# Kernel tuning notes

Hardware: AMD Instinct MI355X
Metric: run time of the kernel (lower is better)

## Reference

```python
import jax, jax.numpy as jnp
import numpy as np
from jax import lax


def _conv1d(x, w):
    # x: (B, L, C), w: (K, C, C), SAME padding (flax nnx.Conv default)
    return lax.conv_general_dilated(x, w, (1,), 'SAME', dimension_numbers=('NWC', 'WIO', 'NWC'))


def _message_passing(x, w, vertical, reverse):
    # x: (B, H, W, C). Sequential SCNN update along H (vertical) or W (horizontal):
    #   slice_i += relu(conv1d(slice_{i-1}))
    if not vertical:
        x = jnp.swapaxes(x, 1, 2)  # scan axis -> axis 1
    if reverse:
        x = x[:, ::-1]
    first = x[:, 0]                       # (B, Wd, C)
    rest = jnp.moveaxis(x[:, 1:], 1, 0)   # (L-1, B, Wd, C)

    def step(prev, row):
        new = row + jax.nn.relu(_conv1d(prev, w))
        return new, new

    _, out = lax.scan(step, first, rest)
    x = jnp.concatenate([first[:, None], jnp.moveaxis(out, 0, 1)], axis=1)
    if reverse:
        x = x[:, ::-1]
    if not vertical:
        x = jnp.swapaxes(x, 1, 2)
    return x


def _bn(x, scale, bias, eps=1e-5):
    # flax nnx.BatchNorm in training mode: batch stats over (B, H, W)
    mean = x.mean((0, 1, 2))
    var = x.var((0, 1, 2))
    return (x - mean) * lax.rsqrt(var + eps) * scale + bias


def reference(features, w_conv1, bn1_scale, bn1_bias, w_conv2, bn2_scale, bn2_bias,
              w_mp_vf, w_mp_vr, w_mp_hf, w_mp_hr, w_seg, b_seg,
              w_fc1, b_fc1, w_fc2, b_fc2):
    dn = ('NHWC', 'HWIO', 'NHWC')
    # dilated 3x3 conv (pad 4, dilation 4) -> BN -> relu
    x = lax.conv_general_dilated(features, w_conv1, (1, 1), [(4, 4), (4, 4)],
                                 rhs_dilation=(4, 4), dimension_numbers=dn)
    x = jax.nn.relu(_bn(x, bn1_scale, bn1_bias))
    # 1x1 conv -> BN -> relu
    x = lax.conv_general_dilated(x, w_conv2, (1, 1), 'SAME', dimension_numbers=dn)
    x = jax.nn.relu(_bn(x, bn2_scale, bn2_bias))
    # four SCNN message-passing directions (sequential scans)
    x = _message_passing(x, w_mp_vf, True, False)
    x = _message_passing(x, w_mp_vr, True, True)
    x = _message_passing(x, w_mp_hf, False, False)
    x = _message_passing(x, w_mp_hr, False, True)
    # seg head: dropout (deterministic -> identity) + 1x1 conv with bias
    x = lax.conv_general_dilated(x, w_seg, (1, 1), 'SAME', dimension_numbers=dn) + b_seg
    b, h, w, f = x.shape
    logits_seg = jax.image.resize(x, (b, h * 8, w * 8, f), method='linear')
    # existence head: softmax -> avg_pool 2x2 -> flatten -> MLP
    p = jax.nn.softmax(x, axis=-1)
    p = p.reshape(b, h // 2, 2, w // 2, 2, f).mean((2, 4))
    p = p.reshape(b, -1)  # (B, (h/2)*(w/2)*f) = (B, 4500)
    z = jax.nn.relu(p @ w_fc1 + b_fc1)
    logits_ext = z @ w_fc2 + b_fc2
    return logits_seg, logits_ext


def setup_inputs() -> dict:
    key = jax.random.key(0)
    ks = jax.random.split(key, 10)
    B, H, W, C = 16, 36, 100, 512
    n_lanes = 4
    s = 0.05
    return {
        'features': jax.random.normal(ks[0], (B, H, W, C), jnp.float32),
        'w_conv1': jax.random.normal(ks[1], (3, 3, 512, 1024), jnp.float32) * s,
        'bn1_scale': jnp.ones((1024,), jnp.float32),
        'bn1_bias': jnp.zeros((1024,), jnp.float32),
        'w_conv2': jax.random.normal(ks[2], (1, 1, 1024, 128), jnp.float32) * s,
        'bn2_scale': jnp.ones((128,), jnp.float32),
        'bn2_bias': jnp.zeros((128,), jnp.float32),
        'w_mp_vf': jax.random.normal(ks[3], (9, 128, 128), jnp.float32) * 0.02,
        'w_mp_vr': jax.random.normal(ks[4], (9, 128, 128), jnp.float32) * 0.02,
        'w_mp_hf': jax.random.normal(ks[5], (9, 128, 128), jnp.float32) * 0.02,
        'w_mp_hr': jax.random.normal(ks[6], (9, 128, 128), jnp.float32) * 0.02,
        'w_seg': jax.random.normal(ks[7], (1, 1, 128, n_lanes + 1), jnp.float32) * s,
        'b_seg': jnp.zeros((n_lanes + 1,), jnp.float32),
        'w_fc1': jax.random.normal(ks[8], (4500, 128), jnp.float32) * s,
        'b_fc1': jnp.zeros((128,), jnp.float32),
        'w_fc2': jax.random.normal(ks[9], (128, n_lanes), jnp.float32) * s,
        'b_fc2': jnp.zeros((n_lanes,), jnp.float32),
    }
```

## Files before the change

kernel.cpp:

```cpp
#include <hip/hip_runtime.h>
#include <hip/hip_bf16.h>

#define NB 16
#define NPOS 57600

typedef short bf16x8 __attribute__((ext_vector_type(8)));
typedef float f32x4 __attribute__((ext_vector_type(4)));

__device__ __forceinline__ float bf2f(unsigned short u) {
  union { unsigned int i; float f; } c; c.i = ((unsigned int)u) << 16; return c.f;
}
__device__ __forceinline__ unsigned short f2bf(float f) {
  union { float f; unsigned int i; } c; c.f = f;
  unsigned int x = c.i;
  x += 0x7fffu + ((x >> 16) & 1u);
  return (unsigned short)(x >> 16);
}
__device__ __forceinline__ unsigned int pk2(float lo, float hi) {
  return (unsigned int)f2bf(lo) | ((unsigned int)f2bf(hi) << 16);
}

__device__ __forceinline__ void gload_lds16(const void* g, void* l) {
  __builtin_amdgcn_global_load_lds(
      (const __attribute__((address_space(1))) unsigned int*)(g),
      (__attribute__((address_space(3))) unsigned int*)(l), 16, 0, 0);
}

__global__ __launch_bounds__(256) void convert_w1t(const float* __restrict__ w,
                                                   unsigned short* __restrict__ wt)
{
  int idx = blockIdx.x * 256 + threadIdx.x;
  int n = idx & 1023;
  int k0 = (idx >> 10) * 8;
  unsigned int o[4];
#pragma unroll
  for (int j = 0; j < 4; ++j) {
    float lo = w[(long)(k0 + 2*j)     * 1024 + n];
    float hi = w[(long)(k0 + 2*j + 1) * 1024 + n];
    o[j] = pk2(lo, hi);
  }
  *(uint4*)(wt + (long)n * 4608 + k0) = make_uint4(o[0], o[1], o[2], o[3]);
}

__global__ __launch_bounds__(256) void convert_w2t(const float* __restrict__ w,
                                                   unsigned short* __restrict__ wt)
{
  int idx = blockIdx.x * 256 + threadIdx.x;
  int n = idx & 127;
  int k0 = (idx >> 7) * 8;
  unsigned int o[4];
#pragma unroll
  for (int j = 0; j < 4; ++j) {
    float lo = w[(long)(k0 + 2*j)     * 128 + n];
    float hi = w[(long)(k0 + 2*j + 1) * 128 + n];
    o[j] = pk2(lo, hi);
  }
  *(uint4*)(wt + (long)n * 1024 + k0) = make_uint4(o[0], o[1], o[2], o[3]);
}

__global__ __launch_bounds__(256) void convert_wmp(const float* __restrict__ w,
                                                   unsigned short* __restrict__ wt)
{
  int idx = blockIdx.x * 256 + threadIdx.x;
  if (idx >= 18432) return;
  int co = idx & 127;
  int kg = idx >> 7;
  int k0 = kg * 8;
  int tap = k0 >> 7, ci0 = k0 & 127;
  const float* src = w + (long)tap * 16384 + (long)ci0 * 128 + co;
  unsigned int o[4];
#pragma unroll
  for (int j = 0; j < 4; ++j)
    o[j] = pk2(src[(2*j) * 128], src[(2*j+1) * 128]);
  *(uint4*)(wt + (long)co * 1152 + k0) = make_uint4(o[0], o[1], o[2], o[3]);
}

__global__ __launch_bounds__(256) void pad_features(const float* __restrict__ src,
                                                    unsigned short* __restrict__ dst)
{
  long idx = (long)blockIdx.x * 256 + threadIdx.x;
  if (idx >= 16L * 44 * 108 * 64) return;
  int c8 = (int)(idx & 63);
  long pos = idx >> 6;
  int wp = (int)(pos % 108); pos /= 108;
  int hp = (int)(pos % 44);
  int b  = (int)(pos / 44);
  uint4 o = make_uint4(0u, 0u, 0u, 0u);
  if (hp >= 4 && hp < 40 && wp >= 4 && wp < 104) {
    const float* s = src + (((long)b * 36 + (hp - 4)) * 100 + (wp - 4)) * 512 + c8 * 8;
    float4 v0 = *(const float4*)s;
    float4 v1 = *(const float4*)(s + 4);
    o = make_uint4(pk2(v0.x, v0.y), pk2(v0.z, v0.w), pk2(v1.x, v1.y), pk2(v1.z, v1.w));
  }
  *(uint4*)(dst + (((long)b * 44 + hp) * 108 + wp) * 512 + c8 * 8) = o;
}

__global__ __launch_bounds__(256) void conv1_mfma2(
    const unsigned short* __restrict__ inp,
    const unsigned short* __restrict__ w1t,
    unsigned short* __restrict__ x1)
{
  __shared__ unsigned short Al[128 * 32];
  __shared__ unsigned short Bl[128 * 32];
  const int tid  = threadIdx.x;
  const int lane = tid & 63;
  const int wave = tid >> 6;
  const int wm = wave >> 1, wn = wave & 1;
  const int bid  = blockIdx.x;
  const int nbid = (bid & 7) * 450 + (bid >> 3);
  const int n0 = (nbid & 7) * 128;
  const int m0 = (nbid >> 3) * 128;

  long aoff[2];
  const unsigned short* bsrc[2];
#pragma unroll
  for (int q = 0; q < 2; ++q) {
    int e = q * 256 + tid;
    int row = e >> 2;
    int kl  = (e & 3) * 8;
    int m = m0 + row;
    int w = m % 100, h = (m / 100) % 36, b = m / 3600;
    aoff[q] = (((long)b * 44 + h + 4) * 108 + (w + 4)) * 512 + kl;
    bsrc[q] = w1t + (long)(n0 + row) * 4608 + kl;
  }

  f32x4 acc[4][4];
#pragma unroll
  for (int i = 0; i < 4; ++i)
#pragma unroll
    for (int j = 0; j < 4; ++j) acc[i][j] = (f32x4){0.f, 0.f, 0.f, 0.f};

  const int fr = lane & 15;
  const int fk = (lane >> 4) * 8;
  const unsigned short* Alrd = Al + (wm * 64 + fr) * 32 + fk;
  const unsigned short* Blrd = Bl + (wn * 64 + fr) * 32 + fk;

  for (int k0 = 0; k0 < 4608; k0 += 32) {
    const int tap = k0 >> 9;
    const int ci0 = k0 & 511;
    const int dh = (tap / 3) * 4 - 4, dw = (tap % 3) * 4 - 4;
    const long delta = (long)(dh * 108 + dw) * 512 + ci0;
    __syncthreads();
#pragma unroll
    for (int q = 0; q < 2; ++q) {
      gload_lds16(inp + aoff[q] + delta, Al + (q * 256 + tid) * 8);
      gload_lds16(bsrc[q] + k0,          Bl + (q * 256 + tid) * 8);
    }
    __syncthreads();
    bf16x8 af[4], bfr[4];
#pragma unroll
    for (int m = 0; m < 4; ++m) af[m]  = *(const bf16x8*)(Alrd + m * 16 * 32);
#pragma unroll
    for (int n = 0; n < 4; ++n) bfr[n] = *(const bf16x8*)(Blrd + n * 16 * 32);
#pragma unroll
    for (int m = 0; m < 4; ++m)
#pragma unroll
      for (int n = 0; n < 4; ++n)
        acc[m][n] = __builtin_amdgcn_mfma_f32_16x16x32_bf16(af[m], bfr[n], acc[m][n], 0, 0, 0);
  }
  const int r0 = (lane >> 4) * 4;
#pragma unroll
  for (int m = 0; m < 4; ++m) {
    int row = m0 + wm * 64 + m * 16 + r0;
#pragma unroll
    for (int n = 0; n < 4; ++n) {
      int col = n0 + wn * 64 + n * 16 + fr;
#pragma unroll
      for (int j = 0; j < 4; ++j)
        x1[(long)(row + j) * 1024 + col] = f2bf(acc[m][n][j]);
    }
  }
}

__global__ __launch_bounds__(256) void conv1_mfma(
    const float* __restrict__ in,
    const unsigned short* __restrict__ w1t,
    unsigned short* __restrict__ x1)
{
  __shared__ unsigned short Al[128 * 32];
  __shared__ unsigned short Bl[128 * 32];
  const int tid  = threadIdx.x;
  const int lane = tid & 63;
  const int wave = tid >> 6;
  const int wm = wave >> 1, wn = wave & 1;
  const int m0 = blockIdx.y * 128;
  const int n0 = blockIdx.x * 128;

  int akl[2], ab_[2], ah_[2], aw_[2];
  const unsigned short* bsrc[2];
#pragma unroll
  for (int q = 0; q < 2; ++q) {
    int e = q * 256 + tid;
    int row = e >> 2;
    akl[q]  = (e & 3) * 8;
    int m = m0 + row;
    aw_[q] = m % 100;
    ah_[q] = (m / 100) % 36;
    ab_[q] = m / 3600;
    bsrc[q] = w1t + (long)(n0 + row) * 4608 + akl[q];
  }

  f32x4 acc[4][4];
#pragma unroll
  for (int i = 0; i < 4; ++i)
#pragma unroll
    for (int j = 0; j < 4; ++j) acc[i][j] = (f32x4){0.f, 0.f, 0.f, 0.f};

  const int fr = lane & 15;
  const int fk = (lane >> 4) * 8;
  const unsigned short* Alrd = Al + (wm * 64 + fr) * 32 + fk;
  const unsigned short* Blrd = Bl + (wn * 64 + fr) * 32 + fk;

  for (int k0 = 0; k0 < 4608; k0 += 32) {
    const int tap = k0 >> 9;
    const int ci0 = k0 & 511;
    const int dh = (tap / 3) * 4 - 4, dw = (tap % 3) * 4 - 4;
    unsigned int apk[2][4];
#pragma unroll
    for (int q = 0; q < 2; ++q) {
      int ih = ah_[q] + dh, iw = aw_[q] + dw;
      if ((unsigned)ih < 36u && (unsigned)iw < 100u) {
        const float* s = in + ((((long)ab_[q] * 36 + ih) * 100 + iw) << 9) + ci0 + akl[q];
        float4 v0 = *(const float4*)s;
        float4 v1 = *(const float4*)(s + 4);
        apk[q][0] = pk2(v0.x, v0.y); apk[q][1] = pk2(v0.z, v0.w);
        apk[q][2] = pk2(v1.x, v1.y); apk[q][3] = pk2(v1.z, v1.w);
      } else {
        apk[q][0] = apk[q][1] = apk[q][2] = apk[q][3] = 0u;
      }
    }
    __syncthreads();
#pragma unroll
    for (int q = 0; q < 2; ++q) {
      *(uint4*)(Al + (q * 256 + tid) * 8) = *(uint4*)apk[q];
      gload_lds16(bsrc[q] + k0, Bl + (q * 256 + tid) * 8);
    }
    __syncthreads();
    bf16x8 af[4], bfr[4];
#pragma unroll
    for (int m = 0; m < 4; ++m) af[m]  = *(const bf16x8*)(Alrd + m * 16 * 32);
#pragma unroll
    for (int n = 0; n < 4; ++n) bfr[n] = *(const bf16x8*)(Blrd + n * 16 * 32);
#pragma unroll
    for (int m = 0; m < 4; ++m)
#pragma unroll
      for (int n = 0; n < 4; ++n)
        acc[m][n] = __builtin_amdgcn_mfma_f32_16x16x32_bf16(af[m], bfr[n], acc[m][n], 0, 0, 0);
  }
  const int r0 = (lane >> 4) * 4;
#pragma unroll
  for (int m = 0; m < 4; ++m) {
    int row = m0 + wm * 64 + m * 16 + r0;
#pragma unroll
    for (int n = 0; n < 4; ++n) {
      int col = n0 + wn * 64 + n * 16 + fr;
#pragma unroll
      for (int j = 0; j < 4; ++j)
        x1[(long)(row + j) * 1024 + col] = f2bf(acc[m][n][j]);
    }
  }
}

__global__ __launch_bounds__(256) void gemm_mfma_128(
    const unsigned short* __restrict__ A,
    const unsigned short* __restrict__ Bt,
    float* __restrict__ C, int K)
{
  __shared__ unsigned short Al[128 * 32];
  __shared__ unsigned short Bl[128 * 32];
  const int tid  = threadIdx.x;
  const int lane = tid & 63;
  const int wave = tid >> 6;
  const int wm = wave >> 1, wn = wave & 1;
  const int m0 = blockIdx.x * 128;

  const unsigned short* asrc[2];
  const unsigned short* bsrc[2];
#pragma unroll
  for (int q = 0; q < 2; ++q) {
    int e = q * 256 + tid;
    int row = e >> 2;
    int kl  = (e & 3) * 8;
    asrc[q] = A  + (long)(m0 + row) * K + kl;
    bsrc[q] = Bt + (long)row * K + kl;
  }

  f32x4 acc[4][4];
#pragma unroll
  for (int i = 0; i < 4; ++i)
#pragma unroll
    for (int j = 0; j < 4; ++j) acc[i][j] = (f32x4){0.f, 0.f, 0.f, 0.f};

  const int fr = lane & 15;
  const int fk = (lane >> 4) * 8;
  const unsigned short* Alrd = Al + (wm * 64 + fr) * 32 + fk;
  const unsigned short* Blrd = Bl + (wn * 64 + fr) * 32 + fk;

  for (int k0 = 0; k0 < K; k0 += 32) {
    __syncthreads();
#pragma unroll
    for (int q = 0; q < 2; ++q) {
      gload_lds16(asrc[q] + k0, Al + (q * 256 + tid) * 8);
      gload_lds16(bsrc[q] + k0, Bl + (q * 256 + tid) * 8);
    }
    __syncthreads();
    bf16x8 af[4], bfr[4];
#pragma unroll
    for (int m = 0; m < 4; ++m) af[m]  = *(const bf16x8*)(Alrd + m * 16 * 32);
#pragma unroll
    for (int n = 0; n < 4; ++n) bfr[n] = *(const bf16x8*)(Blrd + n * 16 * 32);
#pragma unroll
    for (int m = 0; m < 4; ++m)
#pragma unroll
      for (int n = 0; n < 4; ++n)
        acc[m][n] = __builtin_amdgcn_mfma_f32_16x16x32_bf16(af[m], bfr[n], acc[m][n], 0, 0, 0);
  }
  const int r0 = (lane >> 4) * 4;
#pragma unroll
  for (int m = 0; m < 4; ++m) {
    int row = m0 + wm * 64 + m * 16 + r0;
#pragma unroll
    for (int n = 0; n < 4; ++n) {
      int col = wn * 64 + n * 16 + fr;
#pragma unroll
      for (int j = 0; j < 4; ++j)
        C[(long)(row + j) * 128 + col] = acc[m][n][j];
    }
  }
}

__global__ __launch_bounds__(256) void stats1(const unsigned short* __restrict__ x1,
                                              float* __restrict__ sum, float* __restrict__ ssq)
{
  const int tid = threadIdx.x;
  const int c0 = tid * 4;
  float s0=0,s1=0,s2=0,s3=0,q0=0,q1=0,q2=0,q3=0;
  for (int r = blockIdx.x; r < NPOS; r += gridDim.x) {
    uint2 v = *(const uint2*)(x1 + (long)r * 1024 + c0);
    float f0 = bf2f(v.x & 0xffffu), f1 = bf2f(v.x >> 16);
    float f2 = bf2f(v.y & 0xffffu), f3 = bf2f(v.y >> 16);
    s0 += f0; q0 += f0*f0;  s1 += f1; q1 += f1*f1;
    s2 += f2; q2 += f2*f2;  s3 += f3; q3 += f3*f3;
  }
  atomicAdd(&sum[c0+0], s0); atomicAdd(&ssq[c0+0], q0);
  atomicAdd(&sum[c0+1], s1); atomicAdd(&ssq[c0+1], q1);
  atomicAdd(&sum[c0+2], s2); atomicAdd(&ssq[c0+2], q2);
  atomicAdd(&sum[c0+3], s3); atomicAdd(&ssq[c0+3], q3);
}

__global__ void finalize_bn(const float* __restrict__ sum, const float* __restrict__ ssq,
                            const float* __restrict__ scale, const float* __restrict__ bias,
                            float* __restrict__ ab, int C, float invN)
{
  int c = blockIdx.x * blockDim.x + threadIdx.x;
  if (c >= C) return;
  float mean = sum[c] * invN;
  float var  = ssq[c] * invN - mean * mean;
  float a = scale[c] * rsqrtf(var + 1e-5f);
  ab[c] = a;
  ab[C + c] = bias[c] - mean * a;
}

__global__ __launch_bounds__(256) void bnrelu_x1(unsigned short* __restrict__ x1,
                                                 const float* __restrict__ ab)
{
  long base = ((long)blockIdx.x * 256 + threadIdx.x) * 8;
  int c0 = (int)(base & 1023);
  uint4 v = *(uint4*)(x1 + base);
  unsigned int w[4] = {v.x, v.y, v.z, v.w};
  unsigned int o[4];
#pragma unroll
  for (int j = 0; j < 4; ++j) {
    int c = c0 + j * 2;
    float lo = bf2f((unsigned short)(w[j] & 0xffffu));
    float hi = bf2f((unsigned short)(w[j] >> 16));
    lo = fmaxf(fmaf(lo, ab[c],     ab[1024 + c]),     0.f);
    hi = fmaxf(fmaf(hi, ab[c + 1], ab[1024 + c + 1]), 0.f);
    o[j] = pk2(lo, hi);
  }
  *(uint4*)(x1 + base) = make_uint4(o[0], o[1], o[2], o[3]);
}

__global__ __launch_bounds__(256) void stats2(const float* __restrict__ x2,
                                              float* __restrict__ sum, float* __restrict__ ssq)
{
  const int c = threadIdx.x & 127;
  const int g = threadIdx.x >> 7;
  float s = 0.f, q = 0.f;
  for (int r = blockIdx.x * 2 + g; r < NPOS; r += gridDim.x * 2) {
    float v = x2[(long)r * 128 + c];
    s += v; q += v * v;
  }
  atomicAdd(&sum[c], s); atomicAdd(&ssq[c], q);
}

__global__ __launch_bounds__(256) void apply_bn(float* __restrict__ x, const float* __restrict__ ab)
{
  int idx = (blockIdx.x * 256 + threadIdx.x) * 4;
  if (idx >= NPOS * 128) return;
  int c = idx & 127;
  float4 v = *(float4*)(x + idx);
  v.x = fmaxf(fmaf(v.x, ab[c+0], ab[128+c+0]), 0.f);
  v.y = fmaxf(fmaf(v.y, ab[c+1], ab[128+c+1]), 0.f);
  v.z = fmaxf(fmaf(v.z, ab[c+2], ab[128+c+2]), 0.f);
  v.w = fmaxf(fmaf(v.w, ab[c+3], ab[128+c+3]), 0.f);
  *(float4*)(x + idx) = v;
}

#define MPROWS 120
#define MPBUF (MPROWS * 128)
template<int MT, int MH>
__global__ __launch_bounds__(512, 2) void mp_fused2(
    float* __restrict__ x2, const unsigned short* __restrict__ wt,
    const int L, const int posStride, const int rowStride,
    const int i0, const int di, const int nsteps)
{
  __shared__ unsigned short rowbuf[2 * MPBUF];
  __shared__ float xch[MT * 8 * 16 * 17];
  const int tid  = threadIdx.x;
  const int lane = tid & 63;
  const int wave = tid >> 6;
  const int ng   = wave & 3;
  const int kh   = wave >> 2;
  const int fr   = lane & 15;
  const int ks   = lane >> 4;
  float* xb = x2 + (long)blockIdx.x * 460800;

  for (int i = tid; i < (2 * MPBUF) / 8; i += 512)
    *(uint4*)(rowbuf + i * 8) = make_uint4(0u, 0u, 0u, 0u);

  const unsigned short* wb = wt + (long)(ng * 32 + fr) * 1152 + kh * 576 + ks * 8;
  bf16x8 bfrag[2][18];
#pragma unroll
  for (int nt = 0; nt < 2; ++nt)
#pragma unroll
    for (int kk = 0; kk < 18; ++kk)
      bfrag[nt][kk] = *(const bf16x8*)(wb + nt * 16 * 1152 + kk * 32);

  __syncthreads();
  for (int e = tid * 4; e < L * 128; e += 2048) {
    int w = e >> 7, c = e & 127;
    float4 v = *(const float4*)(xb + (long)i0 * rowStride + (long)w * posStride + c);
    int br = w + 4;
    int byte = (br * 256 + c * 2) ^ ((br & 7) << 4);
    *(uint2*)((char*)rowbuf + byte) = make_uint2(pk2(v.x, v.y), pk2(v.z, v.w));
  }
  __syncthreads();

#define MP_EPI(mt)                                                             \
  _Pragma("unroll")                                                            \
  for (int nt = 0; nt < 2; ++nt) {                                             \
    const int col = ng * 32 + nt * 16 + fr;                                    \
    const float* src = &xch[(((mt) * 8 + ng * 2 + nt) * 16) * 17];             \
    _Pragma("unroll")                                                          \
    for (int j = 0; j < 4; ++j) {                                              \
      const int m = (mt) * 16 + ks * 4 + j;                                    \
      if (m < L) {                                                             \
        float v = acc[mt][nt][j] + src[(ks * 4 + j) * 17 + fr];                \
        long off = (long)i * rowStride + (long)m * posStride + col;            \
        float nv = xb[off] + fmaxf(v, 0.f);                                    \
        xb[off] = nv;                                                          \
        int br = m + 4;                                                        \
        int byte = (br * 256 + col * 2) ^ ((br & 7) << 4);                     \
        *(unsigned short*)(nxtb + byte) = f2bf(nv);                            \
      }                                                                        \
    }                                                                          \
  }

  for (int s = 1; s <= nsteps; ++s) {
    const char* curb = (const char*)rowbuf + (((s & 1) ^ 1) * MPBUF) * 2;
    char* nxtb = (char*)rowbuf + ((s & 1) * MPBUF) * 2;
    const int i = i0 + s * di;

    f32x4 acc[MT][2];
#pragma unroll
    for (int mt = 0; mt < MT; ++mt) {
      acc[mt][0] = (f32x4){0.f, 0.f, 0.f, 0.f};
      acc[mt][1] = (f32x4){0.f, 0.f, 0.f, 0.f};
    }

#pragma unroll
    for (int kk = 0; kk < 18; ++kk) {
      const int k0 = kh * 576 + kk * 32;
      const int tap = k0 >> 7;
      const int colb = ((k0 & 127) + ks * 8) * 2;
      const int br0 = fr + tap;
      const int byte0 = (br0 * 256 + colb) ^ ((br0 & 7) << 4);
#pragma unroll
      for (int mt = 0; mt < MT; ++mt) {
        bf16x8 af = *(const bf16x8*)(curb + byte0 + mt * 4096);
        acc[mt][0] = __builtin_amdgcn_mfma_f32_16x16x32_bf16(af, bfrag[0][kk], acc[mt][0], 0, 0, 0);
        acc[mt][1] = __builtin_amdgcn_mfma_f32_16x16x32_bf16(af, bfrag[1][kk], acc[mt][1], 0, 0, 0);
      }
    }

    if (kh == 0) {
#pragma unroll
      for (int mt = MH; mt < MT; ++mt) {
#pragma unroll
        for (int nt = 0; nt < 2; ++nt) {
          float* dst = &xch[((mt * 8 + ng * 2 + nt) * 16) * 17];
#pragma unroll
          for (int j = 0; j < 4; ++j)
            dst[(ks * 4 + j) * 17 + fr] = acc[mt][nt][j];
        }
      }
    } else {
#pragma unroll
      for (int mt = 0; mt < MH; ++mt) {
#pragma unroll
        for (int nt = 0; nt < 2; ++nt) {
          float* dst = &xch[((mt * 8 + ng * 2 + nt) * 16) * 17];
#pragma unroll
          for (int j = 0; j < 4; ++j)
            dst[(ks * 4 + j) * 17 + fr] = acc[mt][nt][j];
        }
      }
    }
    __syncthreads();
    if (kh == 0) {
#pragma unroll
      for (int mt = 0; mt < MH; ++mt) { MP_EPI(mt) }
    } else {
#pragma unroll
      for (int mt = MH; mt < MT; ++mt) { MP_EPI(mt) }
    }
    __syncthreads();
  }
#undef MP_EPI
}

__global__ __launch_bounds__(256) void seg_head(
    const float* __restrict__ xn, const float* __restrict__ w_seg,
    const float* __restrict__ b_seg, float* __restrict__ logits)
{
  __shared__ float ws[128 * 5];
  __shared__ float xs[32][129];
  const int tid = threadIdx.x;
  for (int i = tid; i < 640; i += 256) ws[i] = w_seg[i];
  const int pos0 = blockIdx.x * 32;
  for (int idx = tid; idx < 32 * 32; idx += 256) {
    int r = idx >> 5, q = idx & 31;
    float4 v = *(const float4*)(xn + (long)(pos0 + r) * 128 + q * 4);
    xs[r][q*4+0]=v.x; xs[r][q*4+1]=v.y; xs[r][q*4+2]=v.z; xs[r][q*4+3]=v.w;
  }
  __syncthreads();
  int r = tid >> 3, f = tid & 7;
  if (f < 5) {
    float acc = b_seg[f];
#pragma unroll 4
    for (int ci = 0; ci < 128; ++ci) acc = fmaf(xs[r][ci], ws[ci*5 + f], acc);
    logits[(long)(pos0 + r) * 5 + f] = acc;
  }
}

__global__ __launch_bounds__(256) void softpool(const float* __restrict__ logits, float* __restrict__ p)
{
  int idx = blockIdx.x * 256 + threadIdx.x;
  if (idx >= 16 * 18 * 50) return;
  int ww = idx % 50, hh = (idx / 50) % 18, b = idx / 900;
  float avg[5] = {0,0,0,0,0};
#pragma unroll
  for (int i = 0; i < 2; ++i)
#pragma unroll
    for (int j = 0; j < 2; ++j) {
      const float* L = logits + ((long)((b*36 + hh*2 + i) * 100) + ww*2 + j) * 5;
      float l0=L[0], l1=L[1], l2=L[2], l3=L[3], l4=L[4];
      float m = fmaxf(fmaxf(fmaxf(l0,l1), fmaxf(l2,l3)), l4);
      float e0=expf(l0-m), e1=expf(l1-m), e2=expf(l2-m), e3=expf(l3-m), e4=expf(l4-m);
      float inv = 1.f / (e0+e1+e2+e3+e4);
      avg[0] += e0*inv; avg[1] += e1*inv; avg[2] += e2*inv; avg[3] += e3*inv; avg[4] += e4*inv;
    }
  float* dst = p + (long)b * 4500 + (hh * 50 + ww) * 5;
#pragma unroll
  for (int f = 0; f < 5; ++f) dst[f] = avg[f] * 0.25f;
}

__global__ __launch_bounds__(128) void fc1_kernel(
    const float* __restrict__ p, const float* __restrict__ w,
    const float* __restrict__ bias, float* __restrict__ z)
{
  __shared__ float ps[4500];
  const int b = blockIdx.x, tid = threadIdx.x;
  for (int i = tid; i < 4500; i += 128) ps[i] = p[(long)b * 4500 + i];
  __syncthreads();
  float acc = bias[tid];
#pragma unroll 4
  for (int m = 0; m < 4500; ++m) acc = fmaf(ps[m], w[(long)m * 128 + tid], acc);
  z[b * 128 + tid] = fmaxf(acc, 0.f);
}

__global__ void fc2_kernel(const float* __restrict__ z, const float* __restrict__ w,
                           const float* __restrict__ bias, float* __restrict__ out)
{
  int t = threadIdx.x;
  if (t >= 64) return;
  int b = t >> 2, j = t & 3;
  float acc = bias[j];
#pragma unroll 4
  for (int n = 0; n < 128; ++n) acc = fmaf(z[b*128 + n], w[n*4 + j], acc);
  out[b*4 + j] = acc;
}

__global__ __launch_bounds__(256) void resize_bilinear(
    const float* __restrict__ logits, float* __restrict__ out)
{
  int idx = blockIdx.x * 256 + threadIdx.x;
  if (idx >= 18432000) return;
  int f = idx % 5;
  int t = idx / 5;
  int ow = t % 800; t /= 800;
  int oh = t % 288;
  int b = t / 288;
  float sh = (oh + 0.5f) * 0.125f - 0.5f;
  float sw = (ow + 0.5f) * 0.125f - 0.5f;
  int h0 = (int)floorf(sh); float fh = sh - (float)h0;
  int w0 = (int)floorf(sw); float fw = sw - (float)w0;
  int h1 = min(h0 + 1, 35); h0 = max(h0, 0);
  int w1 = min(w0 + 1, 99); w0 = max(w0, 0);
  const float* Lb = logits + (long)b * 36 * 100 * 5 + f;
  float v00 = Lb[(h0*100 + w0)*5], v01 = Lb[(h0*100 + w1)*5];
  float v10 = Lb[(h1*100 + w0)*5], v11 = Lb[(h1*100 + w1)*5];
  float v = (1.f-fh) * ((1.f-fw)*v00 + fw*v01) + fh * ((1.f-fw)*v10 + fw*v11);
  out[idx] = v;
}

extern "C" void kernel_launch(void* const* d_in, const int* in_sizes, int n_in,
                              void* d_out, int out_size, void* d_ws, size_t ws_size,
                              hipStream_t stream)
{
  (void)in_sizes; (void)n_in; (void)out_size;
  const float* features = (const float*)d_in[0];
  const float* w_conv1  = (const float*)d_in[1];
  const float* bn1_s    = (const float*)d_in[2];
  const float* bn1_b    = (const float*)d_in[3];
  const float* w_conv2  = (const float*)d_in[4];
  const float* bn2_s    = (const float*)d_in[5];
  const float* bn2_b    = (const float*)d_in[6];
  const float* w_vf     = (const float*)d_in[7];
  const float* w_vr     = (const float*)d_in[8];
  const float* w_hf     = (const float*)d_in[9];
  const float* w_hr     = (const float*)d_in[10];
  const float* w_seg    = (const float*)d_in[11];
  const float* b_seg    = (const float*)d_in[12];
  const float* w_fc1    = (const float*)d_in[13];
  const float* b_fc1    = (const float*)d_in[14];
  const float* w_fc2    = (const float*)d_in[15];
  const float* b_fc2    = (const float*)d_in[16];

  char* ws = (char*)d_ws;
  unsigned short* x1  = (unsigned short*)ws;
  unsigned short* w1t = (unsigned short*)(ws + 117964800);
  float* x2     = (float*)(ws + 117964800);
  float* logits = (float*)(ws + 147456000);
  unsigned short* wtmp = (unsigned short*)(ws + 147456000);
  float* pbuf   = (float*)(ws + 148608000);
  float* zbuf   = (float*)(ws + 148896000);
  float* stats  = (float*)(ws + 148904192);
  float* ab1    = (float*)(ws + 148913408);
  float* ab2    = (float*)(ws + 148921600);
  unsigned short* w2t = (unsigned short*)(ws + 148922624);
  unsigned short* in_pad = (unsigned short*)(ws + 149184768);
  const bool use_pad = ws_size >= 227041536ULL;
  float* outf   = (float*)d_out;

  hipMemsetAsync(stats, 0, 2304 * sizeof(float), stream);
  convert_w1t<<<2304, 256, 0, stream>>>(w_conv1, w1t);
  convert_w2t<<<64, 256, 0, stream>>>(w_conv2, w2t);
  convert_wmp<<<72, 256, 0, stream>>>(w_vf, wtmp + 0 * 147456);
  convert_wmp<<<72, 256, 0, stream>>>(w_vr, wtmp + 1 * 147456);
  convert_wmp<<<72, 256, 0, stream>>>(w_hf, wtmp + 2 * 147456);
  convert_wmp<<<72, 256, 0, stream>>>(w_hr, wtmp + 3 * 147456);

  if (use_pad) {
    pad_features<<<19008, 256, 0, stream>>>(features, in_pad);
    conv1_mfma2<<<3600, 256, 0, stream>>>(in_pad, w1t, x1);
  } else {
    conv1_mfma<<<dim3(8, 450), 256, 0, stream>>>(features, w1t, x1);
  }
  stats1<<<512, 256, 0, stream>>>(x1, stats, stats + 1024);
  finalize_bn<<<4, 256, 0, stream>>>(stats, stats + 1024, bn1_s, bn1_b, ab1, 1024, 1.0f/57600.0f);
  bnrelu_x1<<<28800, 256, 0, stream>>>(x1, ab1);
  gemm_mfma_128<<<450, 256, 0, stream>>>(x1, w2t, x2, 1024);
  stats2<<<256, 256, 0, stream>>>(x2, stats + 2048, stats + 2176);
  finalize_bn<<<1, 128, 0, stream>>>(stats + 2048, stats + 2176, bn2_s, bn2_b, ab2, 128, 1.0f/57600.0f);
  apply_bn<<<7200, 256, 0, stream>>>(x2, ab2);

  mp_fused2<7,3><<<NB, 512, 0, stream>>>(x2, wtmp + 0 * 147456, 100, 128,   12800, 0,  +1, 35);
  mp_fused2<7,3><<<NB, 512, 0, stream>>>(x2, wtmp + 1 * 147456, 100, 128,   12800, 35, -1, 35);
  mp_fused2<3,1><<<NB, 512, 0, stream>>>(x2, wtmp + 2 * 147456, 36,  12800, 128,   0,  +1, 99);
  mp_fused2<3,1><<<NB, 512, 0, stream>>>(x2, wtmp + 3 * 147456, 36,  12800, 128,   99, -1, 99);

  seg_head<<<1800, 256, 0, stream>>>(x2, w_seg, b_seg, logits);
  softpool<<<57, 256, 0, stream>>>(logits, pbuf);
  fc1_kernel<<<16, 128, 0, stream>>>(pbuf, w_fc1, b_fc1, zbuf);
  fc2_kernel<<<1, 64, 0, stream>>>(zbuf, w_fc2, b_fc2, outf + 18432000);
  resize_bilinear<<<72000, 256, 0, stream>>>(logits, outf);
}
```

Measured before the change: 3.555 ms.

## Split message-passing work over M tiles instead of K halves, stream weights per tap

The sequential message-passing kernel previously split the K dimension across two wave groups and combined partial sums through a shared-memory exchange with an extra barrier each step, while holding all weight fragments in registers. It now splits the output rows (M tiles) between the two wave groups, so each wave accumulates the full K and writes its own epilogue, which removes the exchange buffer and one barrier per step. Weights are reloaded from global/L2 every step with tap-level double buffering rather than kept resident in registers, and the launch bound no longer requests two blocks per CU. The trade-offs are repeated weight traffic on the serial critical path and uneven M splits (4/3 and 2/1) that leave some waves with more MFMA work.

```diff
diff --git a/kernel.cpp b/kernel.cpp
--- a/kernel.cpp
+++ b/kernel.cpp
@@ -409,34 +409,26 @@
 
 #define MPROWS 120
 #define MPBUF (MPROWS * 128)
-template<int MT, int MH>
-__global__ __launch_bounds__(512, 2) void mp_fused2(
+template<int MT, int MG0>
+__global__ __launch_bounds__(512) void mp_fused3(
     float* __restrict__ x2, const unsigned short* __restrict__ wt,
     const int L, const int posStride, const int rowStride,
     const int i0, const int di, const int nsteps)
 {
+  constexpr int MG1 = MT - MG0;
+  constexpr int NMT = (MG0 > MG1) ? MG0 : MG1;
   __shared__ unsigned short rowbuf[2 * MPBUF];
-  __shared__ float xch[MT * 8 * 16 * 17];
   const int tid  = threadIdx.x;
   const int lane = tid & 63;
   const int wave = tid >> 6;
   const int ng   = wave & 3;
-  const int kh   = wave >> 2;
+  const int mg   = wave >> 2;
   const int fr   = lane & 15;
   const int ks   = lane >> 4;
   float* xb = x2 + (long)blockIdx.x * 460800;
 
   for (int i = tid; i < (2 * MPBUF) / 8; i += 512)
     *(uint4*)(rowbuf + i * 8) = make_uint4(0u, 0u, 0u, 0u);
-
-  const unsigned short* wb = wt + (long)(ng * 32 + fr) * 1152 + kh * 576 + ks * 8;
-  bf16x8 bfrag[2][18];
-#pragma unroll
-  for (int nt = 0; nt < 2; ++nt)
-#pragma unroll
-    for (int kk = 0; kk < 18; ++kk)
-      bfrag[nt][kk] = *(const bf16x8*)(wb + nt * 16 * 1152 + kk * 32);
-
   __syncthreads();
   for (int e = tid * 4; e < L * 128; e += 2048) {
     int w = e >> 7, c = e & 127;
@@ -447,18 +439,18 @@
   }
   __syncthreads();
 
-#define MP_EPI(mt)                                                             \
+  const unsigned short* wb = wt + (long)(ng * 32 + fr) * 1152 + ks * 8;
+
+#define MP_EPI(MTA, pi)                                                        \
   _Pragma("unroll")                                                            \
   for (int nt = 0; nt < 2; ++nt) {                                             \
     const int col = ng * 32 + nt * 16 + fr;                                    \
-    const float* src = &xch[(((mt) * 8 + ng * 2 + nt) * 16) * 17];             \
     _Pragma("unroll")                                                          \
     for (int j = 0; j < 4; ++j) {                                              \
-      const int m = (mt) * 16 + ks * 4 + j;                                    \
+      const int m = (MTA) * 16 + ks * 4 + j;                                   \
       if (m < L) {                                                             \
-        float v = acc[mt][nt][j] + src[(ks * 4 + j) * 17 + fr];                \
         long off = (long)i * rowStride + (long)m * posStride + col;            \
-        float nv = xb[off] + fmaxf(v, 0.f);                                    \
+        float nv = xb[off] + fmaxf(acc[pi][nt][j], 0.f);                       \
         xb[off] = nv;                                                          \
         int br = m + 4;                                                        \
         int byte = (br * 256 + col * 2) ^ ((br & 7) << 4);                     \
@@ -472,58 +464,63 @@
     char* nxtb = (char*)rowbuf + ((s & 1) * MPBUF) * 2;
     const int i = i0 + s * di;
 
-    f32x4 acc[MT][2];
-#pragma unroll
-    for (int mt = 0; mt < MT; ++mt) {
+    f32x4 acc[NMT][2];
+#pragma unroll
+    for (int mt = 0; mt < NMT; ++mt) {
       acc[mt][0] = (f32x4){0.f, 0.f, 0.f, 0.f};
       acc[mt][1] = (f32x4){0.f, 0.f, 0.f, 0.f};
     }
 
-#pragma unroll
-    for (int kk = 0; kk < 18; ++kk) {
-      const int k0 = kh * 576 + kk * 32;
-      const int tap = k0 >> 7;
-      const int colb = ((k0 & 127) + ks * 8) * 2;
-      const int br0 = fr + tap;
-      const int byte0 = (br0 * 256 + colb) ^ ((br0 & 7) << 4);
-#pragma unroll
-      for (int mt = 0; mt < MT; ++mt) {
-        bf16x8 af = *(const bf16x8*)(curb + byte0 + mt * 4096);
-        acc[mt][0] = __builtin_amdgcn_mfma_f32_16x16x32_bf16(af, bfrag[0][kk], acc[mt][0], 0, 0, 0);
-        acc[mt][1] = __builtin_amdgcn_mfma_f32_16x16x32_bf16(af, bfrag[1][kk], acc[mt][1], 0, 0, 0);
+    bf16x8 wbuf[2][2][4];
+#pragma unroll
+    for (int nt = 0; nt < 2; ++nt)
+#pragma unroll
+      for (int q = 0; q < 4; ++q)
+        wbuf[0][nt][q] = *(const bf16x8*)(wb + (long)nt * 16 * 1152 + q * 32);
+
+#pragma unroll
+    for (int tap = 0; tap < 9; ++tap) {
+      constexpr int B0 = 0;
+      const int cur = tap & 1;
+      const int nxt = cur ^ 1;
+      if (tap < 8) {
+#pragma unroll
+        for (int nt = 0; nt < 2; ++nt)
+#pragma unroll
+          for (int q = 0; q < 4; ++q)
+            wbuf[nxt][nt][q] =
+              *(const bf16x8*)(wb + (long)nt * 16 * 1152 + (tap + 1) * 128 + q * 32);
       }
-    }
-
-    if (kh == 0) {
-#pragma unroll
-      for (int mt = MH; mt < MT; ++mt) {
-#pragma unroll
-        for (int nt = 0; nt < 2; ++nt) {
-          float* dst = &xch[((mt * 8 + ng * 2 + nt) * 16) * 17];
-#pragma unroll
-          for (int j = 0; j < 4; ++j)
-            dst[(ks * 4 + j) * 17 + fr] = acc[mt][nt][j];
+      (void)B0;
+#pragma unroll
+      for (int q = 0; q < 4; ++q) {
+        const int colb = (q * 32 + ks * 8) * 2;
+        const int br0 = fr + tap;
+        const int byte0 = (br0 * 256 + colb) ^ ((br0 & 7) << 4);
+        if (mg == 0) {
+#pragma unroll
+          for (int mt = 0; mt < MG0; ++mt) {
+            bf16x8 af = *(const bf16x8*)(curb + byte0 + mt * 4096);
+            acc[mt][0] = __builtin_amdgcn_mfma_f32_16x16x32_bf16(af, wbuf[cur][0][q], acc[mt][0], 0, 0, 0);
+            acc[mt][1] = __builtin_amdgcn_mfma_f32_16x16x32_bf16(af, wbuf[cur][1][q], acc[mt][1], 0, 0, 0);
+          }
+        } else {
+#pragma unroll
+          for (int mt = 0; mt < MG1; ++mt) {
+            bf16x8 af = *(const bf16x8*)(curb + byte0 + (MG0 + mt) * 4096);
+            acc[mt][0] = __builtin_amdgcn_mfma_f32_16x16x32_bf16(af, wbuf[cur][0][q], acc[mt][0], 0, 0, 0);
+            acc[mt][1] = __builtin_amdgcn_mfma_f32_16x16x32_bf16(af, wbuf[cur][1][q], acc[mt][1], 0, 0, 0);
+          }
         }
       }
+    }
+
+    if (mg == 0) {
+#pragma unroll
+      for (int mt = 0; mt < MG0; ++mt) { MP_EPI(mt, mt) }
     } else {
 #pragma unroll
-      for (int mt = 0; mt < MH; ++mt) {
-#pragma unroll
-        for (int nt = 0; nt < 2; ++nt) {
-          float* dst = &xch[((mt * 8 + ng * 2 + nt) * 16) * 17];
-#pragma unroll
-          for (int j = 0; j < 4; ++j)
-            dst[(ks * 4 + j) * 17 + fr] = acc[mt][nt][j];
-        }
-      }
-    }
-    __syncthreads();
-    if (kh == 0) {
-#pragma unroll
-      for (int mt = 0; mt < MH; ++mt) { MP_EPI(mt) }
-    } else {
-#pragma unroll
-      for (int mt = MH; mt < MT; ++mt) { MP_EPI(mt) }
+      for (int mt = 0; mt < MG1; ++mt) { MP_EPI(MG0 + mt, mt) }
     }
     __syncthreads();
   }
@@ -686,10 +683,10 @@
   finalize_bn<<<1, 128, 0, stream>>>(stats + 2048, stats + 2176, bn2_s, bn2_b, ab2, 128, 1.0f/57600.0f);
   apply_bn<<<7200, 256, 0, stream>>>(x2, ab2);
 
-  mp_fused2<7,3><<<NB, 512, 0, stream>>>(x2, wtmp + 0 * 147456, 100, 128,   12800, 0,  +1, 35);
-  mp_fused2<7,3><<<NB, 512, 0, stream>>>(x2, wtmp + 1 * 147456, 100, 128,   12800, 35, -1, 35);
-  mp_fused2<3,1><<<NB, 512, 0, stream>>>(x2, wtmp + 2 * 147456, 36,  12800, 128,   0,  +1, 99);
-  mp_fused2<3,1><<<NB, 512, 0, stream>>>(x2, wtmp + 3 * 147456, 36,  12800, 128,   99, -1, 99);
+  mp_fused3<7,4><<<NB, 512, 0, stream>>>(x2, wtmp + 0 * 147456, 100, 128,   12800, 0,  +1, 35);
+  mp_fused3<7,4><<<NB, 512, 0, stream>>>(x2, wtmp + 1 * 147456, 100, 128,   12800, 35, -1, 35);
+  mp_fused3<3,2><<<NB, 512, 0, stream>>>(x2, wtmp + 2 * 147456, 36,  12800, 128,   0,  +1, 99);
+  mp_fused3<3,2><<<NB, 512, 0, stream>>>(x2, wtmp + 3 * 147456, 36,  12800, 128,   99, -1, 99);
 
   seg_head<<<1800, 256, 0, stream>>>(x2, w_seg, b_seg, logits);
   softpool<<<57, 256, 0, stream>>>(logits, pbuf);
```

Measured after the change: 5.997 ms. 68.7% more time.

## Halve message-passing block to 4 waves, each computing 64 output channels

Applied to the files above, without the earlier changes.

The SCNN message-passing kernel drops from 8 waves to 4 per block. Each wave now covers 64 output columns (4 N-tiles) and one K half, so every A fragment read from LDS feeds 4 MFMAs instead of 2, which cuts LDS traffic per MFMA. Weight fragments are no longer held in registers for the whole kernel; they are reloaded from global memory/cache at every K step, to make room for the larger accumulator set. The intent is to lower LDS and barrier overhead in this latency-bound sequential scan, but with half the waves there is less latency hiding and extra weight loads every step.

```diff
diff --git a/kernel.cpp b/kernel.cpp
--- a/kernel.cpp
+++ b/kernel.cpp
@@ -409,36 +409,27 @@
 
 #define MPROWS 120
 #define MPBUF (MPROWS * 128)
-template<int MT, int MH>
-__global__ __launch_bounds__(512, 2) void mp_fused2(
+template<int MT, int ME0>
+__global__ __launch_bounds__(256) void mp_fused5(
     float* __restrict__ x2, const unsigned short* __restrict__ wt,
     const int L, const int posStride, const int rowStride,
     const int i0, const int di, const int nsteps)
 {
   __shared__ unsigned short rowbuf[2 * MPBUF];
-  __shared__ float xch[MT * 8 * 16 * 17];
+  __shared__ float xch[MT][2][4][16][17];
   const int tid  = threadIdx.x;
   const int lane = tid & 63;
   const int wave = tid >> 6;
-  const int ng   = wave & 3;
-  const int kh   = wave >> 2;
+  const int ng   = wave & 1;
+  const int kg   = wave >> 1;
   const int fr   = lane & 15;
   const int ks   = lane >> 4;
   float* xb = x2 + (long)blockIdx.x * 460800;
 
-  for (int i = tid; i < (2 * MPBUF) / 8; i += 512)
+  for (int i = tid; i < (2 * MPBUF) / 8; i += 256)
     *(uint4*)(rowbuf + i * 8) = make_uint4(0u, 0u, 0u, 0u);
-
-  const unsigned short* wb = wt + (long)(ng * 32 + fr) * 1152 + kh * 576 + ks * 8;
-  bf16x8 bfrag[2][18];
-#pragma unroll
-  for (int nt = 0; nt < 2; ++nt)
-#pragma unroll
-    for (int kk = 0; kk < 18; ++kk)
-      bfrag[nt][kk] = *(const bf16x8*)(wb + nt * 16 * 1152 + kk * 32);
-
   __syncthreads();
-  for (int e = tid * 4; e < L * 128; e += 2048) {
+  for (int e = tid * 4; e < L * 128; e += 1024) {
     int w = e >> 7, c = e & 127;
     float4 v = *(const float4*)(xb + (long)i0 * rowStride + (long)w * posStride + c);
     int br = w + 4;
@@ -447,16 +438,17 @@
   }
   __syncthreads();
 
+  const unsigned short* wb = wt + (long)(ng * 64 + fr) * 1152 + kg * 576 + ks * 8;
+
 #define MP_EPI(mt)                                                             \
   _Pragma("unroll")                                                            \
-  for (int nt = 0; nt < 2; ++nt) {                                             \
-    const int col = ng * 32 + nt * 16 + fr;                                    \
-    const float* src = &xch[(((mt) * 8 + ng * 2 + nt) * 16) * 17];             \
+  for (int nt = 0; nt < 4; ++nt) {                                             \
+    const int col = ng * 64 + nt * 16 + fr;                                    \
     _Pragma("unroll")                                                          \
     for (int j = 0; j < 4; ++j) {                                              \
       const int m = (mt) * 16 + ks * 4 + j;                                    \
       if (m < L) {                                                             \
-        float v = acc[mt][nt][j] + src[(ks * 4 + j) * 17 + fr];                \
+        float v = acc[mt][nt][j] + xch[mt][ng][nt][ks * 4 + j][fr];            \
         long off = (long)i * rowStride + (long)m * posStride + col;            \
         float nv = xb[off] + fmaxf(v, 0.f);                                    \
         xb[off] = nv;                                                          \
@@ -472,58 +464,56 @@
     char* nxtb = (char*)rowbuf + ((s & 1) * MPBUF) * 2;
     const int i = i0 + s * di;
 
-    f32x4 acc[MT][2];
-#pragma unroll
-    for (int mt = 0; mt < MT; ++mt) {
-      acc[mt][0] = (f32x4){0.f, 0.f, 0.f, 0.f};
-      acc[mt][1] = (f32x4){0.f, 0.f, 0.f, 0.f};
-    }
+    f32x4 acc[MT][4];
+#pragma unroll
+    for (int mt = 0; mt < MT; ++mt)
+#pragma unroll
+      for (int nt = 0; nt < 4; ++nt) acc[mt][nt] = (f32x4){0.f, 0.f, 0.f, 0.f};
 
 #pragma unroll
     for (int kk = 0; kk < 18; ++kk) {
-      const int k0 = kh * 576 + kk * 32;
+      const int k0 = kg * 576 + kk * 32;
       const int tap = k0 >> 7;
       const int colb = ((k0 & 127) + ks * 8) * 2;
+      bf16x8 bf[4];
+#pragma unroll
+      for (int nt = 0; nt < 4; ++nt)
+        bf[nt] = *(const bf16x8*)(wb + (long)nt * 16 * 1152 + kk * 32);
       const int br0 = fr + tap;
       const int byte0 = (br0 * 256 + colb) ^ ((br0 & 7) << 4);
 #pragma unroll
       for (int mt = 0; mt < MT; ++mt) {
         bf16x8 af = *(const bf16x8*)(curb + byte0 + mt * 4096);
-        acc[mt][0] = __builtin_amdgcn_mfma_f32_16x16x32_bf16(af, bfrag[0][kk], acc[mt][0], 0, 0, 0);
-        acc[mt][1] = __builtin_amdgcn_mfma_f32_16x16x32_bf16(af, bfrag[1][kk], acc[mt][1], 0, 0, 0);
+#pragma unroll
+        for (int nt = 0; nt < 4; ++nt)
+          acc[mt][nt] = __builtin_amdgcn_mfma_f32_16x16x32_bf16(af, bf[nt], acc[mt][nt], 0, 0, 0);
       }
     }
 
-    if (kh == 0) {
-#pragma unroll
-      for (int mt = MH; mt < MT; ++mt) {
-#pragma unroll
-        for (int nt = 0; nt < 2; ++nt) {
-          float* dst = &xch[((mt * 8 + ng * 2 + nt) * 16) * 17];
+    if (kg == 0) {
+#pragma unroll
+      for (int mt = ME0; mt < MT; ++mt)
+#pragma unroll
+        for (int nt = 0; nt < 4; ++nt)
 #pragma unroll
           for (int j = 0; j < 4; ++j)
-            dst[(ks * 4 + j) * 17 + fr] = acc[mt][nt][j];
-        }
-      }
+            xch[mt][ng][nt][ks * 4 + j][fr] = acc[mt][nt][j];
     } else {
 #pragma unroll
-      for (int mt = 0; mt < MH; ++mt) {
-#pragma unroll
-        for (int nt = 0; nt < 2; ++nt) {
-          float* dst = &xch[((mt * 8 + ng * 2 + nt) * 16) * 17];
+      for (int mt = 0; mt < ME0; ++mt)
+#pragma unroll
+        for (int nt = 0; nt < 4; ++nt)
 #pragma unroll
           for (int j = 0; j < 4; ++j)
-            dst[(ks * 4 + j) * 17 + fr] = acc[mt][nt][j];
-        }
-      }
-    }
-    __syncthreads();
-    if (kh == 0) {
-#pragma unroll
-      for (int mt = 0; mt < MH; ++mt) { MP_EPI(mt) }
+            xch[mt][ng][nt][ks * 4 + j][fr] = acc[mt][nt][j];
+    }
+    __syncthreads();
+    if (kg == 0) {
+#pragma unroll
+      for (int mt = 0; mt < ME0; ++mt) { MP_EPI(mt) }
     } else {
 #pragma unroll
-      for (int mt = MH; mt < MT; ++mt) { MP_EPI(mt) }
+      for (int mt = ME0; mt < MT; ++mt) { MP_EPI(mt) }
     }
     __syncthreads();
   }
@@ -686,10 +676,10 @@
   finalize_bn<<<1, 128, 0, stream>>>(stats + 2048, stats + 2176, bn2_s, bn2_b, ab2, 128, 1.0f/57600.0f);
   apply_bn<<<7200, 256, 0, stream>>>(x2, ab2);
 
-  mp_fused2<7,3><<<NB, 512, 0, stream>>>(x2, wtmp + 0 * 147456, 100, 128,   12800, 0,  +1, 35);
-  mp_fused2<7,3><<<NB, 512, 0, stream>>>(x2, wtmp + 1 * 147456, 100, 128,   12800, 35, -1, 35);
-  mp_fused2<3,1><<<NB, 512, 0, stream>>>(x2, wtmp + 2 * 147456, 36,  12800, 128,   0,  +1, 99);
-  mp_fused2<3,1><<<NB, 512, 0, stream>>>(x2, wtmp + 3 * 147456, 36,  12800, 128,   99, -1, 99);
+  mp_fused5<7,4><<<NB, 256, 0, stream>>>(x2, wtmp + 0 * 147456, 100, 128,   12800, 0,  +1, 35);
+  mp_fused5<7,4><<<NB, 256, 0, stream>>>(x2, wtmp + 1 * 147456, 100, 128,   12800, 35, -1, 35);
+  mp_fused5<3,2><<<NB, 256, 0, stream>>>(x2, wtmp + 2 * 147456, 36,  12800, 128,   0,  +1, 99);
+  mp_fused5<3,2><<<NB, 256, 0, stream>>>(x2, wtmp + 3 * 147456, 36,  12800, 128,   99, -1, 99);
 
   seg_head<<<1800, 256, 0, stream>>>(x2, w_seg, b_seg, logits);
   softpool<<<57, 256, 0, stream>>>(logits, pbuf);
```

Measured after the change: 4.997 ms. 1.41x slower.

## Double message-passing block to 1024 threads with one N-tile per wave

Applied to the files above, without the earlier changes.

The SCNN message-passing kernel now runs 16 waves per block instead of 8. Each wave owns a single 16-column output tile, where it previously owned two. Weight fragments are no longer held in registers for the whole kernel; they are loaded from global memory (likely cache-resident) inside the k-loop on every step. The epilogue split between the two K-halves is rebalanced (MH 3→4, 1→2). The goal is more parallel waves and lower register pressure on the latency-bound sequential scan, at the cost of repeated weight loads and a heavier barrier with more waves.

```diff
diff --git a/kernel.cpp b/kernel.cpp
--- a/kernel.cpp
+++ b/kernel.cpp
@@ -410,7 +410,7 @@
 #define MPROWS 120
 #define MPBUF (MPROWS * 128)
 template<int MT, int MH>
-__global__ __launch_bounds__(512, 2) void mp_fused2(
+__global__ __launch_bounds__(1024) void mp_fused6(
     float* __restrict__ x2, const unsigned short* __restrict__ wt,
     const int L, const int posStride, const int rowStride,
     const int i0, const int di, const int nsteps)
@@ -420,25 +420,16 @@
   const int tid  = threadIdx.x;
   const int lane = tid & 63;
   const int wave = tid >> 6;
-  const int ng   = wave & 3;
-  const int kh   = wave >> 2;
+  const int ng   = wave & 7;
+  const int kh   = wave >> 3;
   const int fr   = lane & 15;
   const int ks   = lane >> 4;
   float* xb = x2 + (long)blockIdx.x * 460800;
 
-  for (int i = tid; i < (2 * MPBUF) / 8; i += 512)
+  for (int i = tid; i < (2 * MPBUF) / 8; i += 1024)
     *(uint4*)(rowbuf + i * 8) = make_uint4(0u, 0u, 0u, 0u);
-
-  const unsigned short* wb = wt + (long)(ng * 32 + fr) * 1152 + kh * 576 + ks * 8;
-  bf16x8 bfrag[2][18];
-#pragma unroll
-  for (int nt = 0; nt < 2; ++nt)
-#pragma unroll
-    for (int kk = 0; kk < 18; ++kk)
-      bfrag[nt][kk] = *(const bf16x8*)(wb + nt * 16 * 1152 + kk * 32);
-
   __syncthreads();
-  for (int e = tid * 4; e < L * 128; e += 2048) {
+  for (int e = tid * 4; e < L * 128; e += 4096) {
     int w = e >> 7, c = e & 127;
     float4 v = *(const float4*)(xb + (long)i0 * rowStride + (long)w * posStride + c);
     int br = w + 4;
@@ -447,16 +438,17 @@
   }
   __syncthreads();
 
+  const unsigned short* wb = wt + (long)(ng * 16 + fr) * 1152 + kh * 576 + ks * 8;
+
 #define MP_EPI(mt)                                                             \
-  _Pragma("unroll")                                                            \
-  for (int nt = 0; nt < 2; ++nt) {                                             \
-    const int col = ng * 32 + nt * 16 + fr;                                    \
-    const float* src = &xch[(((mt) * 8 + ng * 2 + nt) * 16) * 17];             \
+  {                                                                            \
+    const int col = ng * 16 + fr;                                              \
+    const float* src = &xch[((mt) * 8 + ng) * 16 * 17];                        \
     _Pragma("unroll")                                                          \
     for (int j = 0; j < 4; ++j) {                                              \
       const int m = (mt) * 16 + ks * 4 + j;                                    \
       if (m < L) {                                                             \
-        float v = acc[mt][nt][j] + src[(ks * 4 + j) * 17 + fr];                \
+        float v = acc[mt][j] + src[(ks * 4 + j) * 17 + fr];                    \
         long off = (long)i * rowStride + (long)m * posStride + col;            \
         float nv = xb[off] + fmaxf(v, 0.f);                                    \
         xb[off] = nv;                                                          \
@@ -472,49 +464,40 @@
     char* nxtb = (char*)rowbuf + ((s & 1) * MPBUF) * 2;
     const int i = i0 + s * di;
 
-    f32x4 acc[MT][2];
-#pragma unroll
-    for (int mt = 0; mt < MT; ++mt) {
-      acc[mt][0] = (f32x4){0.f, 0.f, 0.f, 0.f};
-      acc[mt][1] = (f32x4){0.f, 0.f, 0.f, 0.f};
-    }
+    f32x4 acc[MT];
+#pragma unroll
+    for (int mt = 0; mt < MT; ++mt) acc[mt] = (f32x4){0.f, 0.f, 0.f, 0.f};
 
 #pragma unroll
     for (int kk = 0; kk < 18; ++kk) {
       const int k0 = kh * 576 + kk * 32;
       const int tap = k0 >> 7;
       const int colb = ((k0 & 127) + ks * 8) * 2;
+      bf16x8 bf = *(const bf16x8*)(wb + kk * 32);
       const int br0 = fr + tap;
       const int byte0 = (br0 * 256 + colb) ^ ((br0 & 7) << 4);
 #pragma unroll
       for (int mt = 0; mt < MT; ++mt) {
         bf16x8 af = *(const bf16x8*)(curb + byte0 + mt * 4096);
-        acc[mt][0] = __builtin_amdgcn_mfma_f32_16x16x32_bf16(af, bfrag[0][kk], acc[mt][0], 0, 0, 0);
-        acc[mt][1] = __builtin_amdgcn_mfma_f32_16x16x32_bf16(af, bfrag[1][kk], acc[mt][1], 0, 0, 0);
+        acc[mt] = __builtin_amdgcn_mfma_f32_16x16x32_bf16(af, bf, acc[mt], 0, 0, 0);
       }
     }
 
     if (kh == 0) {
 #pragma unroll
       for (int mt = MH; mt < MT; ++mt) {
-#pragma unroll
-        for (int nt = 0; nt < 2; ++nt) {
-          float* dst = &xch[((mt * 8 + ng * 2 + nt) * 16) * 17];
-#pragma unroll
-          for (int j = 0; j < 4; ++j)
-            dst[(ks * 4 + j) * 17 + fr] = acc[mt][nt][j];
-        }
+        float* dst = &xch[(mt * 8 + ng) * 16 * 17];
+#pragma unroll
+        for (int j = 0; j < 4; ++j)
+          dst[(ks * 4 + j) * 17 + fr] = acc[mt][j];
       }
     } else {
 #pragma unroll
       for (int mt = 0; mt < MH; ++mt) {
-#pragma unroll
-        for (int nt = 0; nt < 2; ++nt) {
-          float* dst = &xch[((mt * 8 + ng * 2 + nt) * 16) * 17];
-#pragma unroll
-          for (int j = 0; j < 4; ++j)
-            dst[(ks * 4 + j) * 17 + fr] = acc[mt][nt][j];
-        }
+        float* dst = &xch[(mt * 8 + ng) * 16 * 17];
+#pragma unroll
+        for (int j = 0; j < 4; ++j)
+          dst[(ks * 4 + j) * 17 + fr] = acc[mt][j];
       }
     }
     __syncthreads();
@@ -686,10 +669,10 @@
   finalize_bn<<<1, 128, 0, stream>>>(stats + 2048, stats + 2176, bn2_s, bn2_b, ab2, 128, 1.0f/57600.0f);
   apply_bn<<<7200, 256, 0, stream>>>(x2, ab2);
 
-  mp_fused2<7,3><<<NB, 512, 0, stream>>>(x2, wtmp + 0 * 147456, 100, 128,   12800, 0,  +1, 35);
-  mp_fused2<7,3><<<NB, 512, 0, stream>>>(x2, wtmp + 1 * 147456, 100, 128,   12800, 35, -1, 35);
-  mp_fused2<3,1><<<NB, 512, 0, stream>>>(x2, wtmp + 2 * 147456, 36,  12800, 128,   0,  +1, 99);
-  mp_fused2<3,1><<<NB, 512, 0, stream>>>(x2, wtmp + 3 * 147456, 36,  12800, 128,   99, -1, 99);
+  mp_fused6<7,4><<<NB, 1024, 0, stream>>>(x2, wtmp + 0 * 147456, 100, 128,   12800, 0,  +1, 35);
+  mp_fused6<7,4><<<NB, 1024, 0, stream>>>(x2, wtmp + 1 * 147456, 100, 128,   12800, 35, -1, 35);
+  mp_fused6<3,2><<<NB, 1024, 0, stream>>>(x2, wtmp + 2 * 147456, 36,  12800, 128,   0,  +1, 99);
+  mp_fused6<3,2><<<NB, 1024, 0, stream>>>(x2, wtmp + 3 * 147456, 36,  12800, 128,   99, -1, 99);
 
   seg_head<<<1800, 256, 0, stream>>>(x2, w_seg, b_seg, logits);
   softpool<<<57, 256, 0, stream>>>(logits, pbuf);
```

Measured after the change: 3.835 ms. +7.9%, slower.
